# Performance work log

Hardware: AMD Instinct MI355X
Metric: run time of the kernel (lower is better)

## Reference

```python
import jax, jax.numpy as jnp
import numpy as np

T, B, I, H = 1024, 64, 1024, 1024


def setup_inputs() -> dict:
    key = jax.random.key(0)
    ks = jax.random.split(key, 7)
    s = 1.0 / np.sqrt(H)  # uniform_(-sqrt(k), sqrt(k)) with k = 1/hidden_size
    return {
        "x": jax.random.normal(ks[0], (T, B, I), dtype=jnp.float32),
        "W_ih": jax.random.normal(ks[1], (4 * H, I), dtype=jnp.float32) * s,
        "W_hh": jax.random.normal(ks[2], (4 * H, H), dtype=jnp.float32) * s,
        "b_ih": jax.random.normal(ks[3], (4 * H,), dtype=jnp.float32) * s,
        "b_hh": jax.random.normal(ks[4], (4 * H,), dtype=jnp.float32) * s,
        "h0": jax.random.uniform(ks[5], (B, H), dtype=jnp.float32, minval=-s, maxval=s),
        "c0": jax.random.uniform(ks[6], (B, H), dtype=jnp.float32, minval=-s, maxval=s),
    }


def reference(x, W_ih, W_hh, b_ih, b_hh, h0, c0):
    # Precompute input projections for all timesteps in one big GEMM: [T,B,4H]
    x_proj = jnp.einsum("tbi,gi->tbg", x, W_ih) + b_ih + b_hh

    def step(carry, xp_t):
        h, c = carry
        gates = xp_t + h @ W_hh.T  # [B, 4H]
        i, f, g, o = jnp.split(gates, 4, axis=-1)  # torch LSTMCell gate order
        i = jax.nn.sigmoid(i)
        f = jax.nn.sigmoid(f)
        g = jnp.tanh(g)
        o = jax.nn.sigmoid(o)
        c_new = f * c + i * g
        h_new = o * jnp.tanh(c_new)
        return (h_new, c_new), h_new

    (h_T, c_T), out = jax.lax.scan(step, (h0, c0), x_proj)
    return out, h_T, c_T  # out: [T, B, H]
```

## Files before the change

### kernel.cpp

```cpp
#include <hip/hip_runtime.h>

typedef unsigned short u16;
typedef __attribute__((ext_vector_type(8))) __bf16 bf16x8;
typedef __attribute__((ext_vector_type(4))) float f32x4;

#define NWG 256
#define CHUNK 64
#define NCHUNK 16

__device__ __forceinline__ u16 f2b(float f) {
  union { float f; unsigned u; } v; v.f = f;
  unsigned r = (v.u + 0x7fffu + ((v.u >> 16) & 1u)) >> 16;
  return (u16)r;
}
__device__ __forceinline__ float b2f(u16 u) {
  union { unsigned u; float f; } v; v.u = ((unsigned)u) << 16;
  return v.f;
}
__device__ __forceinline__ float sig(float x) { return 1.0f / (1.0f + __expf(-x)); }
__device__ __forceinline__ float tanh_(float x) { return 2.0f / (1.0f + __expf(-2.0f * x)) - 1.0f; }

__global__ __launch_bounds__(256) void prep_kernel(
    const float* __restrict__ W_ih, const float* __restrict__ W_hh,
    const float* __restrict__ b_ih, const float* __restrict__ b_hh,
    const float* __restrict__ h0, const float* __restrict__ c0,
    u16* __restrict__ Wc, float* __restrict__ bias,
    u16* __restrict__ hbuf, float* __restrict__ cst)
{
  const int tid = threadIdx.x;
  const int blk = blockIdx.x;
  {
    const float4 a = *reinterpret_cast<const float4*>(W_ih + (size_t)blk * 1024 + tid * 4);
    const float4 b = *reinterpret_cast<const float4*>(W_hh + (size_t)blk * 1024 + tid * 4);
    u16* dst = Wc + (size_t)blk * 2048;
    *reinterpret_cast<ushort4*>(dst + tid * 4) =
        make_ushort4(f2b(a.x), f2b(a.y), f2b(a.z), f2b(a.w));
    *reinterpret_cast<ushort4*>(dst + 1024 + tid * 4) =
        make_ushort4(f2b(b.x), f2b(b.y), f2b(b.z), f2b(b.w));
  }
  if (blk < 16) {
    int i = blk * 256 + tid;
    bias[i] = b_ih[i] + b_hh[i];
  } else if (blk < 80) {
    int row = blk - 16, k = tid * 4;
    float4 v = *reinterpret_cast<const float4*>(h0 + (size_t)row * 1024 + k);
    *reinterpret_cast<ushort4*>(hbuf + (size_t)row * 1024 + k) =
        make_ushort4(f2b(v.x), f2b(v.y), f2b(v.z), f2b(v.w));
  } else if (blk < 144) {
    int row = blk - 80, k = tid * 4;
    *reinterpret_cast<float4*>(cst + (size_t)row * 1024 + k) =
        *reinterpret_cast<const float4*>(c0 + (size_t)row * 1024 + k);
  }
}

__global__ __launch_bounds__(256) void xproj_kernel(
    const float* __restrict__ xc, const u16* __restrict__ Wc, u16* __restrict__ Xp)
{
  __shared__ __align__(16) u16 As[128][72];
  __shared__ __align__(16) u16 Bs[128][72];
  const int tid = threadIdx.x;
  const int w = tid >> 6, l = tid & 63;
  const int bm = blockIdx.x & 31;
  const int bn = blockIdx.x >> 5;
  const int m0 = bm << 7, n0 = bn << 7;
  const int wm = w & 1, wn = w >> 1;
  const int lr = l & 15, lq = l >> 4;

  f32x4 acc[4][4];
  for (int i = 0; i < 4; ++i)
    for (int j = 0; j < 4; ++j) acc[i][j] = (f32x4){0.f, 0.f, 0.f, 0.f};

  for (int kc = 0; kc < 1024; kc += 64) {
    {
      const int k4 = (tid & 15) << 2;
      const int rb = tid >> 4;
      for (int rp = 0; rp < 128; rp += 16) {
        int row = rp + rb;
        float4 v = *reinterpret_cast<const float4*>(xc + (size_t)(m0 + row) * 1024 + kc + k4);
        unsigned lo = (unsigned)f2b(v.x) | ((unsigned)f2b(v.y) << 16);
        unsigned hi = (unsigned)f2b(v.z) | ((unsigned)f2b(v.w) << 16);
        *reinterpret_cast<uint2*>(&As[row][k4]) = make_uint2(lo, hi);
      }
    }
    {
      const int kk = (tid & 7) << 3;
      const int rb = tid >> 3;
      for (int rp = 0; rp < 128; rp += 32) {
        int row = rp + rb;
        uint4 v = *reinterpret_cast<const uint4*>(Wc + (size_t)(n0 + row) * 2048 + kc + kk);
        *reinterpret_cast<uint4*>(&Bs[row][kk]) = v;
      }
    }
    __syncthreads();
    for (int kb = 0; kb < 2; ++kb) {
      const int ko = kb * 32 + lq * 8;
      bf16x8 af[4], bfr[4];
      for (int i = 0; i < 4; ++i)
        af[i] = *reinterpret_cast<const bf16x8*>(&As[(wm << 6) + (i << 4) + lr][ko]);
      for (int j = 0; j < 4; ++j)
        bfr[j] = *reinterpret_cast<const bf16x8*>(&Bs[(wn << 6) + (j << 4) + lr][ko]);
      for (int i = 0; i < 4; ++i)
        for (int j = 0; j < 4; ++j)
          acc[i][j] = __builtin_amdgcn_mfma_f32_16x16x32_bf16(af[i], bfr[j], acc[i][j], 0, 0, 0);
    }
    __syncthreads();
  }
  for (int i = 0; i < 4; ++i)
    for (int j = 0; j < 4; ++j) {
      int row0 = m0 + (wm << 6) + (i << 4) + lq * 4;
      int coln = n0 + (wn << 6) + (j << 4) + lr;
      for (int r = 0; r < 4; ++r)
        Xp[(size_t)(row0 + r) * 4096 + coln] = f2b(acc[i][j][r]);
    }
}

__global__ __launch_bounds__(256) void scan_kernel(
    const u16* __restrict__ Wc, const u16* __restrict__ Xp,
    u16* __restrict__ hbuf, float* __restrict__ cst, const float* __restrict__ bias,
    float* __restrict__ out, float* __restrict__ outT, float* __restrict__ cT,
    unsigned* __restrict__ arv, unsigned* __restrict__ rel, int t0, int C)
{
  __shared__ __align__(16) u16 Wlds[32 * 64 * 8];
  const int tid = threadIdx.x;
  const int g = blockIdx.x;
  const int w = tid >> 6, l = tid & 63;
  const int n = l & 15, kq = l >> 4;
  const int jj = (g << 2) + (n & 3);
  const int col = ((n >> 2) << 10) + jj;

  for (int i = tid; i < 2048; i += 256) {
    int kb = i >> 6, l2 = i & 63;
    int nn = l2 & 15, kq2 = l2 >> 4;
    int c2 = ((nn >> 2) << 10) + (g << 2) + (nn & 3);
    uint4 v = *reinterpret_cast<const uint4*>(Wc + (size_t)c2 * 2048 + 1024 + kb * 32 + kq2 * 8);
    *reinterpret_cast<uint4*>(&Wlds[i * 8]) = v;
  }
  const float biasv = bias[col];
  const int brow = (w << 4) + (kq << 2);
  float creg[4];
  if (n < 4)
    for (int r = 0; r < 4; ++r) creg[r] = cst[(size_t)(brow + r) * 1024 + jj];
  __syncthreads();

  float xv[4];
  {
    const u16* xpr = Xp + ((size_t)brow << 12) + col;
    for (int r = 0; r < 4; ++r) xv[r] = b2f(xpr[(size_t)r << 12]);
  }

  for (int ts = 0; ts < C; ++ts) {
    const int t = t0 + ts;
    const u16* hs = hbuf + ((t & 1) ? 65536 : 0);
    u16* hd = hbuf + ((t & 1) ? 0 : 65536);
    const u16* arow = hs + (size_t)((w << 4) + n) * 1024 + (kq << 3);
    f32x4 acc0 = {0.f, 0.f, 0.f, 0.f};
    f32x4 acc1 = {0.f, 0.f, 0.f, 0.f};
#pragma unroll
    for (int kb = 0; kb < 32; kb += 2) {
      bf16x8 a0 = *reinterpret_cast<const bf16x8*>(arow + (kb << 5));
      bf16x8 w0 = *reinterpret_cast<const bf16x8*>(&Wlds[((kb << 6) + l) << 3]);
      acc0 = __builtin_amdgcn_mfma_f32_16x16x32_bf16(a0, w0, acc0, 0, 0, 0);
      bf16x8 a1 = *reinterpret_cast<const bf16x8*>(arow + ((kb + 1) << 5));
      bf16x8 w1 = *reinterpret_cast<const bf16x8*>(&Wlds[(((kb + 1) << 6) + l) << 3]);
      acc1 = __builtin_amdgcn_mfma_f32_16x16x32_bf16(a1, w1, acc1, 0, 0, 0);
    }
    float gv[4];
    for (int r = 0; r < 4; ++r) gv[r] = acc0[r] + acc1[r] + xv[r] + biasv;
    const int sb = (l & 48) | (n & 3);
    float fp[4], gp[4], op[4];
    for (int r = 0; r < 4; ++r) {
      fp[r] = __shfl(gv[r], sb + 4);
      gp[r] = __shfl(gv[r], sb + 8);
      op[r] = __shfl(gv[r], sb + 12);
    }
    float hv[4];
    if (n < 4) {
      for (int r = 0; r < 4; ++r) {
        float iv = sig(gv[r]);
        float fv = sig(fp[r]);
        float gg = tanh_(gp[r]);
        float ov = sig(op[r]);
        float cn = fv * creg[r] + iv * gg;
        hv[r] = ov * tanh_(cn);
        creg[r] = cn;
        hd[(size_t)(brow + r) * 1024 + jj] = f2b(hv[r]);
      }
    }

    if (ts + 1 < C) {
      const unsigned v = (unsigned)(t + 1);
      __syncthreads();
      if (g == 0) {
        if (n < 4)
          for (int r = 0; r < 4; ++r)
            out[((size_t)t * 64 + (brow + r)) * 1024 + jj] = hv[r];
        {
          const u16* xpr = Xp + ((size_t)((ts + 1) * 64 + brow) << 12) + col;
          for (int r = 0; r < 4; ++r) xv[r] = b2f(xpr[(size_t)r << 12]);
        }
        if (tid > 0)
          while (__hip_atomic_load(&arv[tid << 5], __ATOMIC_RELAXED, __HIP_MEMORY_SCOPE_AGENT) < v)
            __builtin_amdgcn_s_sleep(1);
        __builtin_amdgcn_fence(__ATOMIC_ACQUIRE, "agent");
        __syncthreads();
        if (tid < 64) {
          __builtin_amdgcn_fence(__ATOMIC_RELEASE, "agent");
          __hip_atomic_store(&rel[tid << 5], v, __ATOMIC_RELAXED, __HIP_MEMORY_SCOPE_AGENT);
        }
      } else {
        if (tid == 0) {
          __builtin_amdgcn_fence(__ATOMIC_RELEASE, "agent");
          __hip_atomic_store(&arv[g << 5], v, __ATOMIC_RELAXED, __HIP_MEMORY_SCOPE_AGENT);
        }
        if (n < 4)
          for (int r = 0; r < 4; ++r)
            out[((size_t)t * 64 + (brow + r)) * 1024 + jj] = hv[r];
        {
          const u16* xpr = Xp + ((size_t)((ts + 1) * 64 + brow) << 12) + col;
          for (int r = 0; r < 4; ++r) xv[r] = b2f(xpr[(size_t)r << 12]);
        }
        if (tid == 0) {
          while (__hip_atomic_load(&rel[(g & 63) << 5], __ATOMIC_RELAXED, __HIP_MEMORY_SCOPE_AGENT) < v)
            __builtin_amdgcn_s_sleep(1);
          __builtin_amdgcn_fence(__ATOMIC_ACQUIRE, "agent");
        }
        __syncthreads();
      }
    } else {
      if (n < 4)
        for (int r = 0; r < 4; ++r)
          out[((size_t)t * 64 + (brow + r)) * 1024 + jj] = hv[r];
    }
    if (t == 1023 && n < 4)
      for (int r = 0; r < 4; ++r) outT[(size_t)(brow + r) * 1024 + jj] = hv[r];
  }
  if (n < 4) {
    for (int r = 0; r < 4; ++r) cst[(size_t)(brow + r) * 1024 + jj] = creg[r];
    if (t0 + C == 1024)
      for (int r = 0; r < 4; ++r) cT[(size_t)(brow + r) * 1024 + jj] = creg[r];
  }
}

extern "C" void kernel_launch(void* const* d_in, const int* in_sizes, int n_in,
                              void* d_out, int out_size, void* d_ws, size_t ws_size,
                              hipStream_t stream)
{
  const float* x    = (const float*)d_in[0];
  const float* W_ih = (const float*)d_in[1];
  const float* W_hh = (const float*)d_in[2];
  const float* b_ih = (const float*)d_in[3];
  const float* b_hh = (const float*)d_in[4];
  const float* h0   = (const float*)d_in[5];
  const float* c0   = (const float*)d_in[6];
  float* out  = (float*)d_out;
  float* outT = out + (size_t)1024 * 64 * 1024;
  float* cT   = outT + 64 * 1024;

  unsigned char* ws = (unsigned char*)d_ws;
  size_t off = 0;
  u16* Wc = (u16*)(ws + off);      off += (size_t)4096 * 2048 * 2;
  float* bias = (float*)(ws + off); off += 4096 * 4;
  u16* hbuf = (u16*)(ws + off);    off += (size_t)2 * 65536 * 2;
  float* cst = (float*)(ws + off); off += (size_t)65536 * 4;
  unsigned* arv = (unsigned*)(ws + off); off += 256 * 32 * 4;
  unsigned* rel = (unsigned*)(ws + off); off += 64 * 32 * 4;
  u16* Xp = (u16*)(ws + off);

  hipMemsetAsync(arv, 0, (256 * 32 + 64 * 32) * 4, stream);
  hipLaunchKernelGGL(prep_kernel, dim3(4096), dim3(256), 0, stream,
                     W_ih, W_hh, b_ih, b_hh, h0, c0, Wc, bias, hbuf, cst);

  for (int c = 0; c < NCHUNK; ++c) {
    int t0 = c * CHUNK;
    hipLaunchKernelGGL(xproj_kernel, dim3(1024), dim3(256), 0, stream,
                       x + (size_t)t0 * 65536, Wc, Xp);
    int C = CHUNK;
    void* args[] = {&Wc, &Xp, &hbuf, &cst, &bias, &out, &outT, &cT, &arv, &rel, &t0, &C};
    if (hipLaunchCooperativeKernel(reinterpret_cast<void*>(scan_kernel),
                                   dim3(NWG), dim3(256), args, 0, stream) != hipSuccess) {
      (void)hipGetLastError();
      hipLaunchKernelGGL(scan_kernel, dim3(NWG), dim3(256), 0, stream,
                         Wc, Xp, hbuf, cst, bias, out, outT, cT, arv, rel, t0, CHUNK);
    }
  }
}
```

Before: 16.72 ms.

## Replace hub-based grid barrier with all-to-all flag polling and pack h stores

The two-level arrive/release barrier through workgroup 0 is replaced by a flat barrier: each workgroup publishes its step counter and every thread polls one of the 256 arrival flags, so the hub round trip disappears. The hidden-state write is packed into one 64-bit store per row via lane shuffles. The recurrent matvec preloads all 32 A fragments and uses four independent accumulators to expose more MFMA parallelism. In exchange, every workgroup now generates 256 polling loads per step, and the new barrier's memory ordering depends on relaxed stores plus an s_waitcnt rather than a release fence.

```diff
diff --git a/kernel.cpp b/kernel.cpp
--- a/kernel.cpp
+++ b/kernel.cpp
@@ -114,11 +114,11 @@
     }
 }
 
-__global__ __launch_bounds__(256) void scan_kernel(
+__global__ __launch_bounds__(256, 1) void scan_kernel(
     const u16* __restrict__ Wc, const u16* __restrict__ Xp,
     u16* __restrict__ hbuf, float* __restrict__ cst, const float* __restrict__ bias,
     float* __restrict__ out, float* __restrict__ outT, float* __restrict__ cT,
-    unsigned* __restrict__ arv, unsigned* __restrict__ rel, int t0, int C)
+    unsigned* __restrict__ arv, int t0, int C)
 {
   __shared__ __align__(16) u16 Wlds[32 * 64 * 8];
   const int tid = threadIdx.x;
@@ -153,19 +153,28 @@
     const u16* hs = hbuf + ((t & 1) ? 65536 : 0);
     u16* hd = hbuf + ((t & 1) ? 0 : 65536);
     const u16* arow = hs + (size_t)((w << 4) + n) * 1024 + (kq << 3);
-    f32x4 acc0 = {0.f, 0.f, 0.f, 0.f};
-    f32x4 acc1 = {0.f, 0.f, 0.f, 0.f};
+    bf16x8 af[32];
 #pragma unroll
-    for (int kb = 0; kb < 32; kb += 2) {
-      bf16x8 a0 = *reinterpret_cast<const bf16x8*>(arow + (kb << 5));
-      bf16x8 w0 = *reinterpret_cast<const bf16x8*>(&Wlds[((kb << 6) + l) << 3]);
-      acc0 = __builtin_amdgcn_mfma_f32_16x16x32_bf16(a0, w0, acc0, 0, 0, 0);
-      bf16x8 a1 = *reinterpret_cast<const bf16x8*>(arow + ((kb + 1) << 5));
-      bf16x8 w1 = *reinterpret_cast<const bf16x8*>(&Wlds[(((kb + 1) << 6) + l) << 3]);
-      acc1 = __builtin_amdgcn_mfma_f32_16x16x32_bf16(a1, w1, acc1, 0, 0, 0);
+    for (int kb = 0; kb < 32; ++kb)
+      af[kb] = *reinterpret_cast<const bf16x8*>(arow + (kb << 5));
+    f32x4 ac0 = {0.f, 0.f, 0.f, 0.f};
+    f32x4 ac1 = {0.f, 0.f, 0.f, 0.f};
+    f32x4 ac2 = {0.f, 0.f, 0.f, 0.f};
+    f32x4 ac3 = {0.f, 0.f, 0.f, 0.f};
+#pragma unroll
+    for (int kb = 0; kb < 32; kb += 4) {
+      ac0 = __builtin_amdgcn_mfma_f32_16x16x32_bf16(
+          af[kb + 0], *reinterpret_cast<const bf16x8*>(&Wlds[(((kb + 0) << 6) + l) << 3]), ac0, 0, 0, 0);
+      ac1 = __builtin_amdgcn_mfma_f32_16x16x32_bf16(
+          af[kb + 1], *reinterpret_cast<const bf16x8*>(&Wlds[(((kb + 1) << 6) + l) << 3]), ac1, 0, 0, 0);
+      ac2 = __builtin_amdgcn_mfma_f32_16x16x32_bf16(
+          af[kb + 2], *reinterpret_cast<const bf16x8*>(&Wlds[(((kb + 2) << 6) + l) << 3]), ac2, 0, 0, 0);
+      ac3 = __builtin_amdgcn_mfma_f32_16x16x32_bf16(
+          af[kb + 3], *reinterpret_cast<const bf16x8*>(&Wlds[(((kb + 3) << 6) + l) << 3]), ac3, 0, 0, 0);
     }
     float gv[4];
-    for (int r = 0; r < 4; ++r) gv[r] = acc0[r] + acc1[r] + xv[r] + biasv;
+    for (int r = 0; r < 4; ++r)
+      gv[r] = ((ac0[r] + ac1[r]) + (ac2[r] + ac3[r])) + xv[r] + biasv;
     const int sb = (l & 48) | (n & 3);
     float fp[4], gp[4], op[4];
     for (int r = 0; r < 4; ++r) {
@@ -183,49 +192,45 @@
         float cn = fv * creg[r] + iv * gg;
         hv[r] = ov * tanh_(cn);
         creg[r] = cn;
-        hd[(size_t)(brow + r) * 1024 + jj] = f2b(hv[r]);
-      }
+      }
+      unsigned long long pw = (unsigned long long)f2b(hv[0])
+                            | ((unsigned long long)f2b(hv[1]) << 16)
+                            | ((unsigned long long)f2b(hv[2]) << 32)
+                            | ((unsigned long long)f2b(hv[3]) << 48);
+      const int tb = l & 48;
+      unsigned long long q0 = __shfl(pw, tb + 0);
+      unsigned long long q1 = __shfl(pw, tb + 1);
+      unsigned long long q2 = __shfl(pw, tb + 2);
+      unsigned long long q3 = __shfl(pw, tb + 3);
+      const int sh = n << 4;
+      unsigned long long st = ((q0 >> sh) & 0xffffull)
+                            | (((q1 >> sh) & 0xffffull) << 16)
+                            | (((q2 >> sh) & 0xffffull) << 32)
+                            | (((q3 >> sh) & 0xffffull) << 48);
+      __hip_atomic_store(
+          reinterpret_cast<unsigned long long*>(hd + (size_t)(brow + n) * 1024 + (g << 2)),
+          st, __ATOMIC_RELAXED, __HIP_MEMORY_SCOPE_AGENT);
     }
 
     if (ts + 1 < C) {
       const unsigned v = (unsigned)(t + 1);
       __syncthreads();
-      if (g == 0) {
-        if (n < 4)
-          for (int r = 0; r < 4; ++r)
-            out[((size_t)t * 64 + (brow + r)) * 1024 + jj] = hv[r];
-        {
-          const u16* xpr = Xp + ((size_t)((ts + 1) * 64 + brow) << 12) + col;
-          for (int r = 0; r < 4; ++r) xv[r] = b2f(xpr[(size_t)r << 12]);
-        }
-        if (tid > 0)
-          while (__hip_atomic_load(&arv[tid << 5], __ATOMIC_RELAXED, __HIP_MEMORY_SCOPE_AGENT) < v)
-            __builtin_amdgcn_s_sleep(1);
-        __builtin_amdgcn_fence(__ATOMIC_ACQUIRE, "agent");
-        __syncthreads();
-        if (tid < 64) {
-          __builtin_amdgcn_fence(__ATOMIC_RELEASE, "agent");
-          __hip_atomic_store(&rel[tid << 5], v, __ATOMIC_RELAXED, __HIP_MEMORY_SCOPE_AGENT);
-        }
-      } else {
-        if (tid == 0) {
-          __builtin_amdgcn_fence(__ATOMIC_RELEASE, "agent");
-          __hip_atomic_store(&arv[g << 5], v, __ATOMIC_RELAXED, __HIP_MEMORY_SCOPE_AGENT);
-        }
-        if (n < 4)
-          for (int r = 0; r < 4; ++r)
-            out[((size_t)t * 64 + (brow + r)) * 1024 + jj] = hv[r];
-        {
-          const u16* xpr = Xp + ((size_t)((ts + 1) * 64 + brow) << 12) + col;
-          for (int r = 0; r < 4; ++r) xv[r] = b2f(xpr[(size_t)r << 12]);
-        }
-        if (tid == 0) {
-          while (__hip_atomic_load(&rel[(g & 63) << 5], __ATOMIC_RELAXED, __HIP_MEMORY_SCOPE_AGENT) < v)
-            __builtin_amdgcn_s_sleep(1);
-          __builtin_amdgcn_fence(__ATOMIC_ACQUIRE, "agent");
-        }
-        __syncthreads();
-      }
+      if (tid == 0) {
+        asm volatile("s_waitcnt vmcnt(0)" ::: "memory");
+        __hip_atomic_store(&arv[g << 5], v, __ATOMIC_RELAXED, __HIP_MEMORY_SCOPE_AGENT);
+      }
+      if (n < 4)
+        for (int r = 0; r < 4; ++r)
+          __hip_atomic_store(&out[((size_t)t * 64 + (brow + r)) * 1024 + jj], hv[r],
+                             __ATOMIC_RELAXED, __HIP_MEMORY_SCOPE_AGENT);
+      {
+        const u16* xpr = Xp + ((size_t)((ts + 1) * 64 + brow) << 12) + col;
+        for (int r = 0; r < 4; ++r) xv[r] = b2f(xpr[(size_t)r << 12]);
+      }
+      while (__hip_atomic_load(&arv[tid << 5], __ATOMIC_RELAXED, __HIP_MEMORY_SCOPE_AGENT) < v)
+        __builtin_amdgcn_s_sleep(1);
+      __syncthreads();
+      __builtin_amdgcn_fence(__ATOMIC_ACQUIRE, "agent");
     } else {
       if (n < 4)
         for (int r = 0; r < 4; ++r)
@@ -263,10 +268,9 @@
   u16* hbuf = (u16*)(ws + off);    off += (size_t)2 * 65536 * 2;
   float* cst = (float*)(ws + off); off += (size_t)65536 * 4;
   unsigned* arv = (unsigned*)(ws + off); off += 256 * 32 * 4;
-  unsigned* rel = (unsigned*)(ws + off); off += 64 * 32 * 4;
   u16* Xp = (u16*)(ws + off);
 
-  hipMemsetAsync(arv, 0, (256 * 32 + 64 * 32) * 4, stream);
+  hipMemsetAsync(arv, 0, 256 * 32 * 4, stream);
   hipLaunchKernelGGL(prep_kernel, dim3(4096), dim3(256), 0, stream,
                      W_ih, W_hh, b_ih, b_hh, h0, c0, Wc, bias, hbuf, cst);
 
@@ -275,12 +279,12 @@
     hipLaunchKernelGGL(xproj_kernel, dim3(1024), dim3(256), 0, stream,
                        x + (size_t)t0 * 65536, Wc, Xp);
     int C = CHUNK;
-    void* args[] = {&Wc, &Xp, &hbuf, &cst, &bias, &out, &outT, &cT, &arv, &rel, &t0, &C};
+    void* args[] = {&Wc, &Xp, &hbuf, &cst, &bias, &out, &outT, &cT, &arv, &t0, &C};
     if (hipLaunchCooperativeKernel(reinterpret_cast<void*>(scan_kernel),
                                    dim3(NWG), dim3(256), args, 0, stream) != hipSuccess) {
       (void)hipGetLastError();
       hipLaunchKernelGGL(scan_kernel, dim3(NWG), dim3(256), 0, stream,
-                         Wc, Xp, hbuf, cst, bias, out, outT, cT, arv, rel, t0, CHUNK);
-    }
-  }
-}
+                         Wc, Xp, hbuf, cst, bias, out, outT, cT, arv, t0, CHUNK);
+    }
+  }
+}
```

After: 16.37 ms. -2.1%, faster.
